# Kernel optimization log

Measured on AMD Instinct MI355X. Metric: run time of the kernel, lower is better.

Reference implementation:

```python
import jax, jax.numpy as jnp
import numpy as np

B = 32768   # batch
F = 32      # per-node feature dim
H = 256     # hidden width
M = 4       # modules per node
OUT = 8     # final output dim
INIT_W = 0.003
B_INIT = 0.1


def _lin(k, din, dout):
    # fanin_init-style uniform weights, bias filled with 0.1 (hidden layers)
    s = 1.0 / np.sqrt(din)
    W = jax.random.uniform(k, (M, din, dout), jnp.float32, -s, s)
    b = jnp.full((M, dout), B_INIT, jnp.float32)
    return W, b


def setup_inputs() -> dict:
    key = jax.random.key(0)
    ks = jax.random.split(key, 16)
    feats = jax.random.normal(ks[0], (B, 4 * F), jnp.float32)
    idx = jax.random.randint(ks[1], (B, 4), 0, M)
    onehots = jax.nn.one_hot(idx, M, dtype=jnp.float32).reshape(B, 4 * M)
    input_val = jnp.concatenate([feats, onehots], axis=1)  # [B,144]

    W00, b00 = _lin(ks[2], F, H)        # node0 post layer 0
    W01, b01 = _lin(ks[3], H, H)        # node0 post layer 1
    Wpre1, bpre1 = _lin(ks[4], F, H)    # node1 pre
    Wpost1, bpost1 = _lin(ks[5], 2 * H, H)  # node1 interface (prev 256 + own 256)
    Wpre2, bpre2 = _lin(ks[6], F, H)
    Wpost2, bpost2 = _lin(ks[7], 2 * H, H)
    Wpre3, bpre3 = _lin(ks[8], F, H)
    Wpost3, bpost3 = _lin(ks[9], 2 * H, H)
    # final output layer: uniform(-init_w, init_w) for W and b, identity act
    Wfin3 = jax.random.uniform(ks[10], (M, H, OUT), jnp.float32, -INIT_W, INIT_W)
    bfin3 = jax.random.uniform(ks[11], (M, OUT), jnp.float32, -INIT_W, INIT_W)
    return dict(input_val=input_val,
                W00=W00, b00=b00, W01=W01, b01=b01,
                Wpre1=Wpre1, bpre1=bpre1, Wpost1=Wpost1, bpost1=bpost1,
                Wpre2=Wpre2, bpre2=bpre2, Wpost2=Wpost2, bpost2=bpost2,
                Wpre3=Wpre3, bpre3=bpre3, Wpost3=Wpost3, bpost3=bpost3,
                Wfin3=Wfin3, bfin3=bfin3)


def _select(h, onehot):
    # per-row pick of the assigned module's output: [B,M,D],[B,M] -> [B,D]
    return jnp.einsum('bmo,bm->bo', h, onehot)


def reference(input_val, W00, b00, W01, b01,
              Wpre1, bpre1, Wpost1, bpost1,
              Wpre2, bpre2, Wpost2, bpost2,
              Wpre3, bpre3, Wpost3, bpost3,
              Wfin3, bfin3):
    feat = lambda j: input_val[:, j * F:(j + 1) * F]
    oh = lambda j: input_val[:, 4 * F + j * M: 4 * F + (j + 1) * M]

    # node 0: two hidden layers, module-dispatched (dense-all-modules + one-hot combine)
    h = jax.nn.relu(jnp.einsum('bi,mio->bmo', feat(0), W00) + b00)
    h = jax.nn.relu(jnp.einsum('bmi,mio->bmo', h, W01) + b01)
    x = _select(h, oh(0))  # [B,H]

    def node(x_prev, fj, ohj, Wpre, bpre, Wpost, bpost):
        hp = jax.nn.relu(jnp.einsum('bi,mio->bmo', fj, Wpre) + bpre)
        # interface layer consumes concat([x_prev, hp]); split the weight to
        # avoid materializing [B,M,2H]
        hq = jax.nn.relu(jnp.einsum('bi,mio->bmo', x_prev, Wpost[:, :H, :])
                         + jnp.einsum('bmi,mio->bmo', hp, Wpost[:, H:, :])
                         + bpost)
        return hq  # [B,M,H]

    x = _select(node(x, feat(1), oh(1), Wpre1, bpre1, Wpost1, bpost1), oh(1))
    x = _select(node(x, feat(2), oh(2), Wpre2, bpre2, Wpost2, bpost2), oh(2))

    h3 = node(x, feat(3), oh(3), Wpre3, bpre3, Wpost3, bpost3)  # [B,M,H]
    out = jnp.einsum('bmi,mio->bmo', h3, Wfin3) + bfin3          # final linear, identity act
    return _select(out, oh(3))  # [B,OUT]
```

## Files before the change

kernel.cpp:

```cpp
#include <hip/hip_runtime.h>

#define NB 32768
#define MAXTILE 768
#define ROWS 64
#define NT 4
#define XHS 536

typedef short s8v __attribute__((ext_vector_type(8)));
typedef short s4v __attribute__((ext_vector_type(4)));
typedef float f4v __attribute__((ext_vector_type(4)));
typedef unsigned short u16;
typedef unsigned short u16x4 __attribute__((ext_vector_type(4)));
typedef unsigned int u32;
typedef unsigned char u8;

__device__ __forceinline__ float bf2f(u16 u) { return __uint_as_float(((u32)u) << 16); }
__device__ __forceinline__ u16 f2bf(float f) {
    u32 x = __float_as_uint(f);
    x += 0x7FFFu + ((x >> 16) & 1u);
    return (u16)(x >> 16);
}
__device__ __forceinline__ s8v ld8(const u16* p) { return *reinterpret_cast<const s8v*>(p); }

#define MFMA16(a, b, c) __builtin_amdgcn_mfma_f32_16x16x32_bf16((a), (b), (c), 0, 0, 0)

template <int N> struct IC { static constexpr int v = N; };

__device__ __forceinline__ void detect_flag(const void* input, int tid, int* shflag)
{
    if (tid < 64) {
        u32 w = ((const u32*)input)[tid];
        u32 h0 = w & 0xFFFFu;
        u32 e0 = (h0 >> 7) & 0xFFu;
        bool plaus = (h0 == 0u) || (e0 >= 96u && e0 <= 143u);
        unsigned long long m = __ballot(plaus);
        if (tid == 0) *shflag = (__popcll(m) >= 48) ? 1 : 0;
    }
}

struct RepArgs {
    const void* W01; const void* Wp[3]; const void* pre[4]; const void* fin;
    const void* bias[9];
    u16 *rPre, *rW01, *rWp[3], *rFin, *cbias;
};

__global__ __launch_bounds__(256) void prepA_kernel(const void* __restrict__ inputv,
                                                    int* __restrict__ hist,
                                                    u16* __restrict__ keyloc,
                                                    RepArgs R)
{
    __shared__ int lcnt[256];
    __shared__ u16 T[8192];
    __shared__ int shmisc;
    int tid = threadIdx.x;
    int b = blockIdx.x;
    detect_flag(inputv, tid, &shmisc);
    __syncthreads();
    int flag = shmisc;

    if (b < 128) {
        lcnt[tid] = 0;
        __syncthreads();
        int row = (b << 8) + tid;
        const u32* in32 = (const u32*)inputv;
        const u16* in16 = (const u16*)inputv;
        int key = 0;
#pragma unroll
        for (int j = 0; j < 4; j++) {
            int base = row * 144 + 128 + j * 4;
            u32 v1, v2, v3;
            if (flag) { v1 = in16[base + 1]; v2 = in16[base + 2]; v3 = in16[base + 3]; }
            else      { v1 = in32[base + 1]; v2 = in32[base + 2]; v3 = in32[base + 3]; }
            int m = v1 ? 1 : (v2 ? 2 : (v3 ? 3 : 0));
            key |= m << (j << 1);
        }
        int loc = atomicAdd(&lcnt[key], 1);
        keyloc[row] = (u16)(key | (loc << 8));
        __syncthreads();
        hist[(b << 8) + tid] = lcnt[tid];
        return;
    }

    int rb = b - 128;
    const void* src = nullptr; u16* dst = nullptr; int K = 0, k0 = 0, mrow = 0;
    if (rb < 32) {
        int m = rb >> 3, s = rb & 7;
        src = R.W01; dst = R.rW01 + (m * 8 + s) * 8192; K = 256; k0 = s * 32; mrow = m;
    } else if (rb < 224) {
        int idx = rb - 32, mat = idx >> 6, r = idx & 63, m = r >> 4, s = r & 15;
        src = R.Wp[mat]; dst = R.rWp[mat] + (m * 16 + s) * 8192; K = 512; k0 = s * 32; mrow = m;
    } else if (rb < 240) {
        int idx = rb - 224, mat = idx >> 2, m = idx & 3;
        src = R.pre[mat]; dst = R.rPre + (mat * 4 + m) * 8192; K = 32; k0 = 0; mrow = m;
    } else if (rb < 244) {
        int m = rb - 240;
        const u16* s16 = (const u16*)R.fin;
        const float* s32 = (const float*)R.fin;
        for (int i = tid; i < 2048; i += 256) {
            int si = (m * 256 + (i >> 3)) * 8 + (i & 7);
            T[i] = flag ? s16[si] : f2bf(s32[si]);
        }
        __syncthreads();
        u16* d = R.rFin + m * 4096;
        for (int i = tid; i < 4096; i += 256) {
            int s = i >> 9, lane = (i >> 3) & 63, j = i & 7;
            int q = lane >> 4, l16 = lane & 15;
            int k = s * 32 + q * 8 + j;
            d[i] = (l16 < 8) ? T[k * 8 + l16] : (u16)0;
        }
        return;
    } else {
        const int sz[9] = {1024,1024,1024,1024,1024,1024,1024,1024,32};
        const int of[9] = {0,1024,2048,3072,4096,5120,6144,7168,8192};
        for (int i = tid; i < 8224; i += 256) {
            int t = i, e = 0;
            while (t >= sz[e]) { t -= sz[e]; e++; }
            R.cbias[of[e] + t] = flag ? ((const u16*)R.bias[e])[t]
                                      : f2bf(((const float*)R.bias[e])[t]);
        }
        return;
    }
    const u16* s16 = (const u16*)src;
    const float* s32 = (const float*)src;
    for (int i = tid; i < 8192; i += 256) {
        int k = i >> 8, n = i & 255;
        int srcIdx = (mrow * K + k0 + k) * 256 + n;
        T[i] = flag ? s16[srcIdx] : f2bf(s32[srcIdx]);
    }
    __syncthreads();
    for (int i = tid; i < 8192; i += 256) {
        int mt = i >> 9, lane = (i >> 3) & 63, j = i & 7;
        int k = ((lane >> 4) << 3) + j, n = (mt << 4) + (lane & 15);
        dst[i] = T[(k << 8) + n];
    }
}

__global__ __launch_bounds__(256) void scatter_kernel(const int* __restrict__ hist,
                                                      const u16* __restrict__ keyloc,
                                                      int* __restrict__ perm,
                                                      int4* __restrict__ tileInfo)
{
    __shared__ int lcnt[256];
    __shared__ int sBase[256];
    int tid = threadIdx.x;
    int b = blockIdx.x;

    int before = 0, tot = 0;
    for (int b2 = 0; b2 < 128; b2++) {
        int h = hist[(b2 << 8) + tid];
        tot += h;
        if (b2 < b) before += h;
    }
    lcnt[tid] = tot;
    __syncthreads();
    for (int off = 1; off < 256; off <<= 1) {
        int v = (tid >= off) ? lcnt[tid - off] : 0;
        __syncthreads();
        lcnt[tid] += v;
        __syncthreads();
    }
    int gbase = lcnt[tid] - tot;
    sBase[tid] = gbase + before;
    __syncthreads();

    if (b == 0) {
        int tiles = (tot + ROWS - 1) / ROWS;
        lcnt[tid] = tiles;
        __syncthreads();
        for (int off = 1; off < 256; off <<= 1) {
            int v = (tid >= off) ? lcnt[tid - off] : 0;
            __syncthreads();
            lcnt[tid] += v;
            __syncthreads();
        }
        int tbase = lcnt[tid] - tiles;
        int ttot = lcnt[255];
        for (int t = 0; t < tiles; t++) {
            int rem = tot - t * ROWS;
            tileInfo[tbase + t] = make_int4(tid, gbase + t * ROWS, rem > ROWS ? ROWS : rem, 0);
        }
        for (int i = ttot + tid; i < MAXTILE; i += 256)
            tileInfo[i] = make_int4(0, 0, 0, 0);
    }

    int row = (b << 8) + tid;
    u32 kl = keyloc[row];
    int key = kl & 255, loc = kl >> 8;
    perm[sBase[key] + loc] = row;
}

struct MainP { const u16 *rPre, *rW01, *rWp1, *rWp2, *rWp3, *rFin, *cbias; };

__global__ __launch_bounds__(512, 4) void main_kernel(
    const void* __restrict__ inRaw,
    const int* __restrict__ perm, const int4* __restrict__ tileInfo,
    MainP P, void* __restrict__ outp)
{
    __shared__ __align__(16) u16 xh[ROWS * XHS];
    __shared__ int rowids[ROWS];
    __shared__ int shflag;

    int tid = threadIdx.x;
    int lane = tid & 63, w = tid >> 6, quad = lane >> 4, l16 = lane & 15;

    int b = blockIdx.x;
    int t = ((b & 7) * (MAXTILE / 8)) + (b >> 3);
    int4 ti = tileInfo[t];
    int key = ti.x, ppos = ti.y, cntIn = ti.z;
    if (cntIn <= 0) return;

    detect_flag(inRaw, tid, &shflag);
    if (tid < ROWS) {
        int g = tid < cntIn ? tid : cntIn - 1;
        rowids[tid] = perm[ppos + g];
    }
    __syncthreads();
    int flag = shflag;
    int rows_[NT];
#pragma unroll
    for (int nt = 0; nt < NT; nt++) rows_[nt] = rowids[nt * 16 + l16];

    const u16* in16 = (const u16*)inRaw;
    const float* in32 = (const float*)inRaw;
    int mt0 = w << 1, mt1 = mt0 + 1;

    f4v acc0[NT], acc1[NT];

    auto gemm_run = [&](auto nc, const u16* Ab, int ks0) {
        constexpr int N = decltype(nc)::v;
        constexpr int D = 4;
        const u16* base0 = Ab + mt0 * 512 + lane * 8;
        const u16* base1 = Ab + mt1 * 512 + lane * 8;
        s8v A0[D], A1[D];
#pragma unroll
        for (int d = 0; d < D && d < N; d++) {
            A0[d] = ld8(base0 + d * 8192);
            A1[d] = ld8(base1 + d * 8192);
        }
        __syncthreads();
#pragma unroll
        for (int s = 0; s < N; s++) {
            s8v c0 = A0[s % D], c1 = A1[s % D];
            if (s + D < N) {
                A0[s % D] = ld8(base0 + (s + D) * 8192);
                A1[s % D] = ld8(base1 + (s + D) * 8192);
            }
#pragma unroll
            for (int nt = 0; nt < NT; nt++) {
                s8v B = ld8(&xh[(nt * 16 + l16) * XHS + (ks0 + s) * 32 + quad * 8]);
                acc0[nt] = MFMA16(c0, B, acc0[nt]);
                acc1[nt] = MFMA16(c1, B, acc1[nt]);
            }
        }
    };

    for (int node = 0; node < 4; node++) {
        int m = (key >> (node << 1)) & 3;

        s8v fb[NT];
#pragma unroll
        for (int nt = 0; nt < NT; nt++) {
            int off = rows_[nt] * 144 + (node << 5) + (quad << 3);
            if (flag) fb[nt] = ld8(in16 + off);
            else {
                f4v f0 = *(const f4v*)(in32 + off);
                f4v f1 = *(const f4v*)(in32 + off + 4);
                s8v r;
#pragma unroll
                for (int j = 0; j < 4; j++) { r[j] = (short)f2bf(f0[j]); r[4 + j] = (short)f2bf(f1[j]); }
                fb[nt] = r;
            }
        }

        const u16* preB = P.rPre + ((node << 2) + m) * 8192;
#pragma unroll
        for (int ci = 0; ci < 2; ci++) {
            int mt = mt0 + ci;
            s8v a = ld8(preB + mt * 512 + lane * 8);
            u16x4 bv = *(const u16x4*)(P.cbias + node * 2048 + m * 256 + mt * 16 + quad * 4);
            f4v bias;
#pragma unroll
            for (int r = 0; r < 4; r++) bias[r] = bf2f(bv[r]);
#pragma unroll
            for (int nt = 0; nt < NT; nt++) {
                f4v c = MFMA16(a, fb[nt], bias);
                s4v p;
#pragma unroll
                for (int r = 0; r < 4; r++) { float v = c[r] > 0.f ? c[r] : 0.f; p[r] = (short)f2bf(v); }
                *(s4v*)&xh[(nt * 16 + l16) * XHS + 256 + mt * 16 + quad * 4] = p;
            }
        }

        {
            u16x4 b0 = *(const u16x4*)(P.cbias + node * 2048 + 1024 + m * 256 + mt0 * 16 + quad * 4);
            u16x4 b1 = *(const u16x4*)(P.cbias + node * 2048 + 1024 + m * 256 + mt1 * 16 + quad * 4);
            f4v f0, f1;
#pragma unroll
            for (int r = 0; r < 4; r++) { f0[r] = bf2f(b0[r]); f1[r] = bf2f(b1[r]); }
#pragma unroll
            for (int nt = 0; nt < NT; nt++) { acc0[nt] = f0; acc1[nt] = f1; }
        }

        if (node == 0) gemm_run(IC<8>{},  P.rW01 + m * 8 * 8192, 8);
        else {
            const u16* WB = (node == 1 ? P.rWp1 : (node == 2 ? P.rWp2 : P.rWp3)) + m * 16 * 8192;
            gemm_run(IC<16>{}, WB, 0);
        }
        __syncthreads();

#pragma unroll
        for (int ci = 0; ci < 2; ci++) {
            int mt = mt0 + ci;
#pragma unroll
            for (int nt = 0; nt < NT; nt++) {
                f4v a = ci ? acc1[nt] : acc0[nt];
                s4v p;
#pragma unroll
                for (int r = 0; r < 4; r++) { float v = a[r] > 0.f ? a[r] : 0.f; p[r] = (short)f2bf(v); }
                *(s4v*)&xh[(nt * 16 + l16) * XHS + mt * 16 + quad * 4] = p;
            }
        }
    }
    __syncthreads();

    if (w < NT) {
        int m3 = (key >> 6) & 3;
        f4v c;
#pragma unroll
        for (int r = 0; r < 4; r++)
            c[r] = (quad < 2) ? bf2f(P.cbias[8192 + m3 * 8 + quad * 4 + r]) : 0.f;
#pragma unroll
        for (int s = 0; s < 8; s++) {
            s8v A = ld8(P.rFin + m3 * 4096 + s * 512 + lane * 8);
            s8v B = ld8(&xh[(w * 16 + l16) * XHS + s * 32 + quad * 8]);
            c = MFMA16(A, B, c);
        }
        int bidx = w * 16 + l16;
        if (quad < 2 && bidx < cntIn) {
            int row = rowids[bidx];
            if (flag) {
                s4v p;
#pragma unroll
                for (int r = 0; r < 4; r++) p[r] = (short)f2bf(c[r]);
                *(s4v*)((u16*)outp + row * 8 + quad * 4) = p;
            } else {
                *(f4v*)((float*)outp + row * 8 + quad * 4) = c;
            }
        }
    }
}

extern "C" void kernel_launch(void* const* d_in, const int* in_sizes, int n_in,
                              void* d_out, int out_size, void* d_ws, size_t ws_size,
                              hipStream_t stream)
{
    (void)in_sizes; (void)n_in; (void)out_size;
    const void* input  = d_in[0];
    const void* W00    = d_in[1];
    const void* b00    = d_in[2];
    const void* W01    = d_in[3];
    const void* b01    = d_in[4];
    const void* Wpre1  = d_in[5];
    const void* bpre1  = d_in[6];
    const void* Wpost1 = d_in[7];
    const void* bpost1 = d_in[8];
    const void* Wpre2  = d_in[9];
    const void* bpre2  = d_in[10];
    const void* Wpost2 = d_in[11];
    const void* bpost2 = d_in[12];
    const void* Wpre3  = d_in[13];
    const void* bpre3  = d_in[14];
    const void* Wpost3 = d_in[15];
    const void* bpost3 = d_in[16];
    const void* Wfin   = d_in[17];
    const void* bfin   = d_in[18];

    char* base = (char*)d_ws;
    size_t off = 0;
    auto alloc = [&](size_t bytes) -> char* {
        char* p = base + off;
        off += (bytes + 255) & ~(size_t)255;
        return p;
    };
    int*  hist      = (int*)alloc(128 * 256 * 4);
    u16*  keyloc    = (u16*)alloc(NB * 2);
    int4* tileInfo  = (int4*)alloc(MAXTILE * 16);
    int*  perm      = (int*)alloc((size_t)NB * 4);
    u16*  cbias    = (u16*)alloc(8224 * 2);
    u16*  rPre     = (u16*)alloc(131072 * 2);
    u16*  rW01     = (u16*)alloc(262144 * 2);
    u16*  rWp1     = (u16*)alloc(524288 * 2);
    u16*  rWp2     = (u16*)alloc(524288 * 2);
    u16*  rWp3     = (u16*)alloc(524288 * 2);
    u16*  rFin     = (u16*)alloc(16384 * 2);
    if (off > ws_size) return;

    RepArgs R;
    R.W01 = W01; R.Wp[0] = Wpost1; R.Wp[1] = Wpost2; R.Wp[2] = Wpost3;
    R.pre[0] = W00; R.pre[1] = Wpre1; R.pre[2] = Wpre2; R.pre[3] = Wpre3;
    R.fin = Wfin;
    R.bias[0] = b00;   R.bias[1] = b01;
    R.bias[2] = bpre1; R.bias[3] = bpost1;
    R.bias[4] = bpre2; R.bias[5] = bpost2;
    R.bias[6] = bpre3; R.bias[7] = bpost3;
    R.bias[8] = bfin;
    R.rPre = rPre; R.rW01 = rW01;
    R.rWp[0] = rWp1; R.rWp[1] = rWp2; R.rWp[2] = rWp3;
    R.rFin = rFin; R.cbias = cbias;

    prepA_kernel<<<373, 256, 0, stream>>>(input, hist, keyloc, R);
    scatter_kernel<<<128, 256, 0, stream>>>(hist, keyloc, perm, tileInfo);

    MainP P;
    P.rPre = rPre; P.rW01 = rW01; P.rWp1 = rWp1; P.rWp2 = rWp2; P.rWp3 = rWp3;
    P.rFin = rFin; P.cbias = cbias;
    main_kernel<<<MAXTILE, 512, 0, stream>>>(input, perm, tileInfo, P, d_out);
}
```

Before: 194.5 us.

## Widen main kernel to 1024 threads, split weight repack, transpose histogram

The main kernel now runs 16 waves per block, each owning one 16-column output tile instead of two, which halves per-thread accumulator and A-fragment registers and shortens the prefetch depth. The weight repack is split into quarter-K blocks (more blocks, smaller LDS tile). The histogram is stored transposed so the scatter kernel can read it with vector loads. Tile-to-block mapping drops the interleaved order. More threads per block raises LDS B-fragment re-reads per MFMA and barrier cost, and 8 blocks of 1024 threads per CU may not fit.

```diff
diff --git a/kernel.cpp b/kernel.cpp
--- a/kernel.cpp
+++ b/kernel.cpp
@@ -45,12 +45,12 @@
 };
 
 __global__ __launch_bounds__(256) void prepA_kernel(const void* __restrict__ inputv,
-                                                    int* __restrict__ hist,
+                                                    int* __restrict__ histT,
                                                     u16* __restrict__ keyloc,
                                                     RepArgs R)
 {
     __shared__ int lcnt[256];
-    __shared__ u16 T[8192];
+    __shared__ u16 T[2048];
     __shared__ int shmisc;
     int tid = threadIdx.x;
     int b = blockIdx.x;
@@ -77,36 +77,45 @@
         int loc = atomicAdd(&lcnt[key], 1);
         keyloc[row] = (u16)(key | (loc << 8));
         __syncthreads();
-        hist[(b << 8) + tid] = lcnt[tid];
+        histT[tid * 128 + b] = lcnt[tid];
         return;
     }
 
     int rb = b - 128;
-    const void* src = nullptr; u16* dst = nullptr; int K = 0, k0 = 0, mrow = 0;
-    if (rb < 32) {
-        int m = rb >> 3, s = rb & 7;
+    const void* src; u16* dst; int K, k0, mrow, kq;
+    if (rb < 128) {
+        int tile = rb >> 2; kq = rb & 3;
+        int m = tile >> 3, s = tile & 7;
         src = R.W01; dst = R.rW01 + (m * 8 + s) * 8192; K = 256; k0 = s * 32; mrow = m;
-    } else if (rb < 224) {
-        int idx = rb - 32, mat = idx >> 6, r = idx & 63, m = r >> 4, s = r & 15;
+    } else if (rb < 896) {
+        int u = rb - 128, mat = u >> 8, r = u & 255;
+        int tile = r >> 2; kq = r & 3;
+        int m = tile >> 4, s = tile & 15;
         src = R.Wp[mat]; dst = R.rWp[mat] + (m * 16 + s) * 8192; K = 512; k0 = s * 32; mrow = m;
-    } else if (rb < 240) {
-        int idx = rb - 224, mat = idx >> 2, m = idx & 3;
+    } else if (rb < 960) {
+        int u = rb - 896;
+        int tile = u >> 2; kq = u & 3;
+        int mat = tile >> 2, m = tile & 3;
         src = R.pre[mat]; dst = R.rPre + (mat * 4 + m) * 8192; K = 32; k0 = 0; mrow = m;
-    } else if (rb < 244) {
-        int m = rb - 240;
+    } else if (rb < 964) {
+        int m = rb - 960;
         const u16* s16 = (const u16*)R.fin;
         const float* s32 = (const float*)R.fin;
-        for (int i = tid; i < 2048; i += 256) {
-            int si = (m * 256 + (i >> 3)) * 8 + (i & 7);
-            T[i] = flag ? s16[si] : f2bf(s32[si]);
-        }
-        __syncthreads();
         u16* d = R.rFin + m * 4096;
-        for (int i = tid; i < 4096; i += 256) {
-            int s = i >> 9, lane = (i >> 3) & 63, j = i & 7;
-            int q = lane >> 4, l16 = lane & 15;
-            int k = s * 32 + q * 8 + j;
-            d[i] = (l16 < 8) ? T[k * 8 + l16] : (u16)0;
+        for (int half = 0; half < 2; half++) {
+            for (int i = tid; i < 1024; i += 256) {
+                int kk = half * 128 + (i >> 3);
+                T[i] = flag ? s16[(m * 256 + kk) * 8 + (i & 7)]
+                            : f2bf(s32[(m * 256 + kk) * 8 + (i & 7)]);
+            }
+            __syncthreads();
+            for (int i = tid; i < 2048; i += 256) {
+                int s = (half << 2) + (i >> 9), lane = (i >> 3) & 63, j = i & 7;
+                int q = lane >> 4, l16 = lane & 15;
+                int k = s * 32 + q * 8 + j;
+                d[s * 512 + lane * 8 + j] = (l16 < 8) ? T[(k - half * 128) * 8 + l16] : (u16)0;
+            }
+            __syncthreads();
         }
         return;
     } else {
@@ -122,20 +131,19 @@
     }
     const u16* s16 = (const u16*)src;
     const float* s32 = (const float*)src;
-    for (int i = tid; i < 8192; i += 256) {
-        int k = i >> 8, n = i & 255;
-        int srcIdx = (mrow * K + k0 + k) * 256 + n;
+    for (int i = tid; i < 2048; i += 256) {
+        int kk = i >> 8, n = i & 255;
+        int srcIdx = (mrow * K + k0 + kq * 8 + kk) * 256 + n;
         T[i] = flag ? s16[srcIdx] : f2bf(s32[srcIdx]);
     }
     __syncthreads();
-    for (int i = tid; i < 8192; i += 256) {
-        int mt = i >> 9, lane = (i >> 3) & 63, j = i & 7;
-        int k = ((lane >> 4) << 3) + j, n = (mt << 4) + (lane & 15);
-        dst[i] = T[(k << 8) + n];
-    }
-}
-
-__global__ __launch_bounds__(256) void scatter_kernel(const int* __restrict__ hist,
+    for (int i = tid; i < 2048; i += 256) {
+        int mt = i >> 7, r = i & 127, l15 = r >> 3, j = i & 7;
+        dst[mt * 512 + kq * 128 + r] = T[j * 256 + mt * 16 + l15];
+    }
+}
+
+__global__ __launch_bounds__(256) void scatter_kernel(const int* __restrict__ histT,
                                                       const u16* __restrict__ keyloc,
                                                       int* __restrict__ perm,
                                                       int4* __restrict__ tileInfo)
@@ -145,11 +153,17 @@
     int tid = threadIdx.x;
     int b = blockIdx.x;
 
-    int before = 0, tot = 0;
-    for (int b2 = 0; b2 < 128; b2++) {
-        int h = hist[(b2 << 8) + tid];
-        tot += h;
-        if (b2 < b) before += h;
+    const int4* hrow = (const int4*)(histT + tid * 128);
+    int tot = 0, before = 0;
+#pragma unroll
+    for (int j = 0; j < 32; j++) {
+        int4 h = hrow[j];
+        int i4 = j << 2;
+        tot += h.x + h.y + h.z + h.w;
+        if (i4 + 0 < b) before += h.x;
+        if (i4 + 1 < b) before += h.y;
+        if (i4 + 2 < b) before += h.z;
+        if (i4 + 3 < b) before += h.w;
     }
     lcnt[tid] = tot;
     __syncthreads();
@@ -191,7 +205,7 @@
 
 struct MainP { const u16 *rPre, *rW01, *rWp1, *rWp2, *rWp3, *rFin, *cbias; };
 
-__global__ __launch_bounds__(512, 4) void main_kernel(
+__global__ __launch_bounds__(1024, 8) void main_kernel(
     const void* __restrict__ inRaw,
     const int* __restrict__ perm, const int4* __restrict__ tileInfo,
     MainP P, void* __restrict__ outp)
@@ -203,9 +217,7 @@
     int tid = threadIdx.x;
     int lane = tid & 63, w = tid >> 6, quad = lane >> 4, l16 = lane & 15;
 
-    int b = blockIdx.x;
-    int t = ((b & 7) * (MAXTILE / 8)) + (b >> 3);
-    int4 ti = tileInfo[t];
+    int4 ti = tileInfo[blockIdx.x];
     int key = ti.x, ppos = ti.y, cntIn = ti.z;
     if (cntIn <= 0) return;
 
@@ -222,34 +234,27 @@
 
     const u16* in16 = (const u16*)inRaw;
     const float* in32 = (const float*)inRaw;
-    int mt0 = w << 1, mt1 = mt0 + 1;
-
-    f4v acc0[NT], acc1[NT];
+    int mt = w;
+
+    f4v acc[NT];
+    s8v fb[NT];
 
     auto gemm_run = [&](auto nc, const u16* Ab, int ks0) {
         constexpr int N = decltype(nc)::v;
-        constexpr int D = 4;
-        const u16* base0 = Ab + mt0 * 512 + lane * 8;
-        const u16* base1 = Ab + mt1 * 512 + lane * 8;
-        s8v A0[D], A1[D];
-#pragma unroll
-        for (int d = 0; d < D && d < N; d++) {
-            A0[d] = ld8(base0 + d * 8192);
-            A1[d] = ld8(base1 + d * 8192);
-        }
+        constexpr int D = 3;
+        const u16* base = Ab + mt * 512 + lane * 8;
+        s8v A[D];
+#pragma unroll
+        for (int d = 0; d < D && d < N; d++) A[d] = ld8(base + d * 8192);
         __syncthreads();
 #pragma unroll
         for (int s = 0; s < N; s++) {
-            s8v c0 = A0[s % D], c1 = A1[s % D];
-            if (s + D < N) {
-                A0[s % D] = ld8(base0 + (s + D) * 8192);
-                A1[s % D] = ld8(base1 + (s + D) * 8192);
-            }
+            s8v c = A[s % D];
+            if (s + D < N) A[s % D] = ld8(base + (s + D) * 8192);
 #pragma unroll
             for (int nt = 0; nt < NT; nt++) {
                 s8v B = ld8(&xh[(nt * 16 + l16) * XHS + (ks0 + s) * 32 + quad * 8]);
-                acc0[nt] = MFMA16(c0, B, acc0[nt]);
-                acc1[nt] = MFMA16(c1, B, acc1[nt]);
+                acc[nt] = MFMA16(c, B, acc[nt]);
             }
         }
     };
@@ -257,7 +262,6 @@
     for (int node = 0; node < 4; node++) {
         int m = (key >> (node << 1)) & 3;
 
-        s8v fb[NT];
 #pragma unroll
         for (int nt = 0; nt < NT; nt++) {
             int off = rows_[nt] * 144 + (node << 5) + (quad << 3);
@@ -272,10 +276,8 @@
             }
         }
 
-        const u16* preB = P.rPre + ((node << 2) + m) * 8192;
-#pragma unroll
-        for (int ci = 0; ci < 2; ci++) {
-            int mt = mt0 + ci;
+        {
+            const u16* preB = P.rPre + ((node << 2) + m) * 8192;
             s8v a = ld8(preB + mt * 512 + lane * 8);
             u16x4 bv = *(const u16x4*)(P.cbias + node * 2048 + m * 256 + mt * 16 + quad * 4);
             f4v bias;
@@ -292,13 +294,12 @@
         }
 
         {
-            u16x4 b0 = *(const u16x4*)(P.cbias + node * 2048 + 1024 + m * 256 + mt0 * 16 + quad * 4);
-            u16x4 b1 = *(const u16x4*)(P.cbias + node * 2048 + 1024 + m * 256 + mt1 * 16 + quad * 4);
-            f4v f0, f1;
-#pragma unroll
-            for (int r = 0; r < 4; r++) { f0[r] = bf2f(b0[r]); f1[r] = bf2f(b1[r]); }
-#pragma unroll
-            for (int nt = 0; nt < NT; nt++) { acc0[nt] = f0; acc1[nt] = f1; }
+            u16x4 bv = *(const u16x4*)(P.cbias + node * 2048 + 1024 + m * 256 + mt * 16 + quad * 4);
+            f4v f0;
+#pragma unroll
+            for (int r = 0; r < 4; r++) f0[r] = bf2f(bv[r]);
+#pragma unroll
+            for (int nt = 0; nt < NT; nt++) acc[nt] = f0;
         }
 
         if (node == 0) gemm_run(IC<8>{},  P.rW01 + m * 8 * 8192, 8);
@@ -309,16 +310,11 @@
         __syncthreads();
 
 #pragma unroll
-        for (int ci = 0; ci < 2; ci++) {
-            int mt = mt0 + ci;
-#pragma unroll
-            for (int nt = 0; nt < NT; nt++) {
-                f4v a = ci ? acc1[nt] : acc0[nt];
-                s4v p;
-#pragma unroll
-                for (int r = 0; r < 4; r++) { float v = a[r] > 0.f ? a[r] : 0.f; p[r] = (short)f2bf(v); }
-                *(s4v*)&xh[(nt * 16 + l16) * XHS + mt * 16 + quad * 4] = p;
-            }
+        for (int nt = 0; nt < NT; nt++) {
+            s4v p;
+#pragma unroll
+            for (int r = 0; r < 4; r++) { float v = acc[nt][r] > 0.f ? acc[nt][r] : 0.f; p[r] = (short)f2bf(v); }
+            *(s4v*)&xh[(nt * 16 + l16) * XHS + mt * 16 + quad * 4] = p;
         }
     }
     __syncthreads();
@@ -382,7 +378,7 @@
         off += (bytes + 255) & ~(size_t)255;
         return p;
     };
-    int*  hist      = (int*)alloc(128 * 256 * 4);
+    int*  histT     = (int*)alloc(256 * 128 * 4);
     u16*  keyloc    = (u16*)alloc(NB * 2);
     int4* tileInfo  = (int4*)alloc(MAXTILE * 16);
     int*  perm      = (int*)alloc((size_t)NB * 4);
@@ -408,11 +404,11 @@
     R.rWp[0] = rWp1; R.rWp[1] = rWp2; R.rWp[2] = rWp3;
     R.rFin = rFin; R.cbias = cbias;
 
-    prepA_kernel<<<373, 256, 0, stream>>>(input, hist, keyloc, R);
-    scatter_kernel<<<128, 256, 0, stream>>>(hist, keyloc, perm, tileInfo);
+    prepA_kernel<<<1093, 256, 0, stream>>>(input, histT, keyloc, R);
+    scatter_kernel<<<128, 256, 0, stream>>>(histT, keyloc, perm, tileInfo);
 
     MainP P;
     P.rPre = rPre; P.rW01 = rW01; P.rWp1 = rWp1; P.rWp2 = rWp2; P.rWp3 = rWp3;
     P.rFin = rFin; P.cbias = cbias;
-    main_kernel<<<MAXTILE, 512, 0, stream>>>(input, perm, tileInfo, P, d_out);
-}
+    main_kernel<<<MAXTILE, 1024, 0, stream>>>(input, perm, tileInfo, P, d_out);
+}
```

Result: slower. 212.3 us (+9.2%).
